# Kernel tuning notes

Hardware: AMD Instinct MI355X
Metric: run time of the kernel (lower is better)

Reference implementation:

```python
import jax, jax.numpy as jnp
import numpy as np

COUPLE_BOOST = 2.0
MARGIN = 1.0
EPS = 1e-6  # both F.normalize eps and F.pairwise_distance eps


def setup_inputs() -> dict:
    key = jax.random.key(0)
    n, d = 8192, 256
    embeddings = jax.random.normal(key, (n, d), dtype=jnp.float32)
    # Alternating couple labels per the is_partner docstring: 0,1,0,1,...
    labels = jnp.tile(jnp.array([0, 1], dtype=jnp.int64), n // 2).reshape(n, 1)
    return {"embeddings": embeddings, "labels": labels}


def reference(embeddings, labels):
    n, d = embeddings.shape
    # F.normalize(p=2, dim=1, eps=1e-6): x / max(||x||, eps)
    norm = jnp.linalg.norm(embeddings, axis=1, keepdims=True)
    e = embeddings / jnp.maximum(norm, EPS)
    # F.pairwise_distance adds eps to the difference: d_ij = ||e_i - e_j + eps||_2
    # ||e_i - e_j + eps*1||^2 = s_i + s_j - 2 G_ij + 2*eps*(r_i - r_j) + d*eps^2
    s = jnp.sum(e * e, axis=1)          # (n,) squared norms
    r = jnp.sum(e, axis=1)              # (n,) row sums
    G = e @ e.T                         # (n, n) gram matrix
    dist2 = (s[:, None] + s[None, :] - 2.0 * G
             + 2.0 * EPS * (r[:, None] - r[None, :]) + d * EPS * EPS)
    dist = jnp.sqrt(jnp.maximum(dist2, 1e-12))

    lab = labels[:, 0]
    idx = jnp.arange(n)
    tril = idx[:, None] > idx[None, :]                  # loop only visits i > j
    same = lab[:, None] == lab[None, :]
    pos_mask = tril & same
    neg_mask = tril & (~same)
    # is_partner with i > j: labels[i]==1 and i == j+1
    partner = (idx[:, None] == idx[None, :] + 1) & (lab[:, None] == 1)
    boost = jnp.where(partner, COUPLE_BOOST, 1.0)

    pos_loss = 0.5 * jnp.square(jnp.maximum(dist - 0.1, 0.0))
    neg_loss = 0.5 * boost * jnp.square(jnp.maximum(MARGIN - dist, 0.0))

    total = (jnp.sum(jnp.where(pos_mask, pos_loss, 0.0))
             + jnp.sum(jnp.where(neg_mask, neg_loss, 0.0)))
    n_comparisons = n * (n - 1) // 2
    return total / n_comparisons
```

## Files before the change

kernel.cpp:

```cpp
#include <hip/hip_runtime.h>
#include <hip/hip_bf16.h>

#define NROWS 8192
#define DIM   256
#define EPSV  1e-6f
#define BM    128
#define BN    128
#define BK    32
#define BKP   40

typedef __bf16 bf16x8 __attribute__((ext_vector_type(8)));
typedef float  f32x4  __attribute__((ext_vector_type(4)));

__global__ __launch_bounds__(256) void normalize_kernel(
    const float* __restrict__ emb, __bf16* __restrict__ Ebf,
    float* __restrict__ P_out, float* __restrict__ Q_out,
    float* __restrict__ out)
{
    if (blockIdx.x == 0 && threadIdx.x == 0) out[0] = 0.0f;

    const int wave = threadIdx.x >> 6;
    const int lane = threadIdx.x & 63;
    const int row  = blockIdx.x * 4 + wave;

    const float4 v = ((const float4*)(emb + row * DIM))[lane];
    float ss = v.x*v.x + v.y*v.y + v.z*v.z + v.w*v.w;
    #pragma unroll
    for (int off = 32; off; off >>= 1) ss += __shfl_xor(ss, off);

    const float inv = 1.0f / fmaxf(sqrtf(ss), EPSV);
    float4 e; e.x = v.x*inv; e.y = v.y*inv; e.z = v.z*inv; e.w = v.w*inv;

    float sp = e.x*e.x + e.y*e.y + e.z*e.z + e.w*e.w;
    float rp = e.x + e.y + e.z + e.w;
    #pragma unroll
    for (int off = 32; off; off >>= 1) {
        sp += __shfl_xor(sp, off);
        rp += __shfl_xor(rp, off);
    }

    union { __bf16 h[4]; uint2 u; } pk;
    pk.h[0] = (__bf16)e.x; pk.h[1] = (__bf16)e.y;
    pk.h[2] = (__bf16)e.z; pk.h[3] = (__bf16)e.w;
    *(uint2*)(Ebf + row * DIM + lane * 4) = pk.u;

    if (lane == 0) {
        const float c = 0.5f * (float)DIM * EPSV * EPSV;
        P_out[row] = sp + 2.0f * EPSV * rp + c;
        Q_out[row] = sp - 2.0f * EPSV * rp + c;
    }
}

__global__ __launch_bounds__(256) void loss_kernel(
    const __bf16* __restrict__ Ebf,
    const float* __restrict__ P_arr, const float* __restrict__ Q_arr,
    const int* __restrict__ lab, float* __restrict__ out)
{
    const int t = blockIdx.x;
    int bi = (int)((sqrtf(8.0f * (float)t + 1.0f) - 1.0f) * 0.5f);
    while ((bi + 1) * (bi + 2) / 2 <= t) ++bi;
    while (bi * (bi + 1) / 2 > t) --bi;
    const int bj = t - bi * (bi + 1) / 2;
    const bool diag = (bi == bj);

    __shared__ __align__(16) __bf16 As[BM * BKP];
    __shared__ __align__(16) __bf16 Bs[BN * BKP];
    __shared__ float sP[BM], sQ[BN];
    __shared__ int   lI[BM], lJ[BN];
    __shared__ float wsum[4];

    const int tid  = threadIdx.x;
    const int wave = tid >> 6;
    const int lane = tid & 63;
    const int i0 = bi * BM, j0 = bj * BN;

    if (tid < 128) {
        sP[tid] = P_arr[i0 + tid]; lI[tid] = lab[i0 + tid];
        sQ[tid] = Q_arr[j0 + tid]; lJ[tid] = lab[j0 + tid];
    }

    f32x4 acc[4][4] = {};
    const int wm = wave >> 1, wn = wave & 1;
    const int quad = lane >> 4, mlane = lane & 15;

    #pragma unroll 1
    for (int kt = 0; kt < DIM / BK; ++kt) {
        const int k0 = kt * BK;
        #pragma unroll
        for (int rr = 0; rr < 2; ++rr) {
            const int c   = tid + rr * 256;
            const int row = c >> 2;
            const int col = (c & 3) * 8;
            *(uint4*)(As + row * BKP + col) =
                *(const uint4*)(Ebf + (size_t)(i0 + row) * DIM + k0 + col);
            *(uint4*)(Bs + row * BKP + col) =
                *(const uint4*)(Ebf + (size_t)(j0 + row) * DIM + k0 + col);
        }
        __syncthreads();

        bf16x8 af[4], bfr[4];
        #pragma unroll
        for (int f = 0; f < 4; ++f) {
            af[f]  = *(const bf16x8*)(As + (wm * 64 + f * 16 + mlane) * BKP + quad * 8);
            bfr[f] = *(const bf16x8*)(Bs + (wn * 64 + f * 16 + mlane) * BKP + quad * 8);
        }
        #pragma unroll
        for (int fa = 0; fa < 4; ++fa)
            #pragma unroll
            for (int fb = 0; fb < 4; ++fb)
                acc[fa][fb] = __builtin_amdgcn_mfma_f32_16x16x32_bf16(
                    af[fa], bfr[fb], acc[fa][fb], 0, 0, 0);
        __syncthreads();
    }

    float qv[4]; int lv[4], gjv[4];
    #pragma unroll
    for (int fb = 0; fb < 4; ++fb) {
        const int jl = wn * 64 + fb * 16 + mlane;
        qv[fb]  = sQ[jl];
        lv[fb]  = lJ[jl];
        gjv[fb] = j0 + jl;
    }

    float lsum = 0.0f;
    #pragma unroll
    for (int fa = 0; fa < 4; ++fa) {
        #pragma unroll
        for (int reg = 0; reg < 4; ++reg) {
            const int il = wm * 64 + fa * 16 + quad * 4 + reg;
            const int gi = i0 + il;
            const float pi = sP[il];
            const int   li = lI[il];
            #pragma unroll
            for (int fb = 0; fb < 4; ++fb) {
                const float g  = acc[fa][fb][reg];
                const float d2 = __builtin_fmaf(-2.0f, g, pi + qv[fb]);
                const float d  = __builtin_amdgcn_sqrtf(fmaxf(d2, 1e-12f));
                const bool same = (li == lv[fb]);
                float tt = same ? (d - 0.1f) : (1.0f - d);
                tt = fmaxf(tt, 0.0f);
                const float w = same ? 0.5f
                                     : ((gi == gjv[fb] + 1 && li == 1) ? 1.0f : 0.5f);
                float contrib = w * tt * tt;
                if (diag) contrib = (gi > gjv[fb]) ? contrib : 0.0f;
                lsum += contrib;
            }
        }
    }

    #pragma unroll
    for (int off = 32; off; off >>= 1) lsum += __shfl_down(lsum, off);
    if (lane == 0) wsum[wave] = lsum;
    __syncthreads();
    if (tid == 0) {
        const float bs = wsum[0] + wsum[1] + wsum[2] + wsum[3];
        const float scale = 1.0f / 33550336.0f;
        atomicAdd(out, bs * scale);
    }
}

extern "C" void kernel_launch(void* const* d_in, const int* in_sizes, int n_in,
                              void* d_out, int out_size, void* d_ws, size_t ws_size,
                              hipStream_t stream)
{
    const float* emb = (const float*)d_in[0];
    const int*   lab = (const int*)d_in[1];
    float*       out = (float*)d_out;

    __bf16* Ebf   = (__bf16*)d_ws;
    float*  P_arr = (float*)((char*)d_ws + (size_t)NROWS * DIM * 2);
    float*  Q_arr = P_arr + NROWS;

    normalize_kernel<<<NROWS / 4, 256, 0, stream>>>(emb, Ebf, P_arr, Q_arr, out);
    loss_kernel<<<64 * 65 / 2, 256, 0, stream>>>(Ebf, P_arr, Q_arr, lab, out);
}
```

Before: 110.1 us.

## Load MFMA fragments directly from global with register double-buffering, drop LDS staging

The loss kernel no longer stages A/B tiles through shared memory with two barriers per k-step. Each wave now loads its bf16x8 fragments straight from global memory and prefetches the next k-slice into registers while the current MFMAs run. Waves whose 64x64 sub-tile lies entirely above the diagonal of a diagonal block skip their work, and P/Q/labels are read from global instead of LDS. The normalize kernel also derives squared norm and row sum from the raw reductions, removing a second shuffle reduction. The trade-off is no cross-wave reuse through LDS, which means more global/L2 traffic and less coalesced loads, plus higher register pressure.

```diff
diff --git a/kernel.cpp b/kernel.cpp
--- a/kernel.cpp
+++ b/kernel.cpp
@@ -4,10 +4,6 @@
 #define NROWS 8192
 #define DIM   256
 #define EPSV  1e-6f
-#define BM    128
-#define BN    128
-#define BK    32
-#define BKP   40
 
 typedef __bf16 bf16x8 __attribute__((ext_vector_type(8)));
 typedef float  f32x4  __attribute__((ext_vector_type(4)));
@@ -25,19 +21,15 @@
 
     const float4 v = ((const float4*)(emb + row * DIM))[lane];
     float ss = v.x*v.x + v.y*v.y + v.z*v.z + v.w*v.w;
+    float rs = v.x + v.y + v.z + v.w;
     #pragma unroll
-    for (int off = 32; off; off >>= 1) ss += __shfl_xor(ss, off);
+    for (int off = 32; off; off >>= 1) {
+        ss += __shfl_xor(ss, off);
+        rs += __shfl_xor(rs, off);
+    }
 
     const float inv = 1.0f / fmaxf(sqrtf(ss), EPSV);
     float4 e; e.x = v.x*inv; e.y = v.y*inv; e.z = v.z*inv; e.w = v.w*inv;
-
-    float sp = e.x*e.x + e.y*e.y + e.z*e.z + e.w*e.w;
-    float rp = e.x + e.y + e.z + e.w;
-    #pragma unroll
-    for (int off = 32; off; off >>= 1) {
-        sp += __shfl_xor(sp, off);
-        rp += __shfl_xor(rp, off);
-    }
 
     union { __bf16 h[4]; uint2 u; } pk;
     pk.h[0] = (__bf16)e.x; pk.h[1] = (__bf16)e.y;
@@ -45,7 +37,9 @@
     *(uint2*)(Ebf + row * DIM + lane * 4) = pk.u;
 
     if (lane == 0) {
-        const float c = 0.5f * (float)DIM * EPSV * EPSV;
+        const float sp = ss * inv * inv;
+        const float rp = rs * inv;
+        const float c  = 0.5f * (float)DIM * EPSV * EPSV;
         P_out[row] = sp + 2.0f * EPSV * rp + c;
         Q_out[row] = sp - 2.0f * EPSV * rp + c;
     }
@@ -63,87 +57,86 @@
     const int bj = t - bi * (bi + 1) / 2;
     const bool diag = (bi == bj);
 
-    __shared__ __align__(16) __bf16 As[BM * BKP];
-    __shared__ __align__(16) __bf16 Bs[BN * BKP];
-    __shared__ float sP[BM], sQ[BN];
-    __shared__ int   lI[BM], lJ[BN];
     __shared__ float wsum[4];
 
     const int tid  = threadIdx.x;
     const int wave = tid >> 6;
     const int lane = tid & 63;
-    const int i0 = bi * BM, j0 = bj * BN;
+    const int i0 = bi * 128, j0 = bj * 128;
 
-    if (tid < 128) {
-        sP[tid] = P_arr[i0 + tid]; lI[tid] = lab[i0 + tid];
-        sQ[tid] = Q_arr[j0 + tid]; lJ[tid] = lab[j0 + tid];
-    }
-
-    f32x4 acc[4][4] = {};
     const int wm = wave >> 1, wn = wave & 1;
     const int quad = lane >> 4, mlane = lane & 15;
 
-    #pragma unroll 1
-    for (int kt = 0; kt < DIM / BK; ++kt) {
-        const int k0 = kt * BK;
-        #pragma unroll
-        for (int rr = 0; rr < 2; ++rr) {
-            const int c   = tid + rr * 256;
-            const int row = c >> 2;
-            const int col = (c & 3) * 8;
-            *(uint4*)(As + row * BKP + col) =
-                *(const uint4*)(Ebf + (size_t)(i0 + row) * DIM + k0 + col);
-            *(uint4*)(Bs + row * BKP + col) =
-                *(const uint4*)(Ebf + (size_t)(j0 + row) * DIM + k0 + col);
-        }
-        __syncthreads();
+    float lsum = 0.0f;
+    const bool skip = diag && (wm < wn);
 
-        bf16x8 af[4], bfr[4];
+    if (!skip) {
+        const __bf16* pA = Ebf + (size_t)(i0 + wm * 64 + mlane) * DIM + quad * 8;
+        const __bf16* pB = Ebf + (size_t)(j0 + wn * 64 + mlane) * DIM + quad * 8;
+
+        f32x4 acc[4][4] = {};
+        bf16x8 a_cur[4], b_cur[4], a_nxt[4], b_nxt[4];
+
         #pragma unroll
         for (int f = 0; f < 4; ++f) {
-            af[f]  = *(const bf16x8*)(As + (wm * 64 + f * 16 + mlane) * BKP + quad * 8);
-            bfr[f] = *(const bf16x8*)(Bs + (wn * 64 + f * 16 + mlane) * BKP + quad * 8);
+            a_cur[f] = *(const bf16x8*)(pA + (size_t)f * 16 * DIM);
+            b_cur[f] = *(const bf16x8*)(pB + (size_t)f * 16 * DIM);
         }
+
         #pragma unroll
-        for (int fa = 0; fa < 4; ++fa)
+        for (int kt = 0; kt < DIM / 32; ++kt) {
+            if (kt < DIM / 32 - 1) {
+                #pragma unroll
+                for (int f = 0; f < 4; ++f) {
+                    a_nxt[f] = *(const bf16x8*)(pA + (size_t)f * 16 * DIM + (kt + 1) * 32);
+                    b_nxt[f] = *(const bf16x8*)(pB + (size_t)f * 16 * DIM + (kt + 1) * 32);
+                }
+            }
             #pragma unroll
-            for (int fb = 0; fb < 4; ++fb)
-                acc[fa][fb] = __builtin_amdgcn_mfma_f32_16x16x32_bf16(
-                    af[fa], bfr[fb], acc[fa][fb], 0, 0, 0);
-        __syncthreads();
-    }
+            for (int fa = 0; fa < 4; ++fa)
+                #pragma unroll
+                for (int fb = 0; fb < 4; ++fb)
+                    acc[fa][fb] = __builtin_amdgcn_mfma_f32_16x16x32_bf16(
+                        a_cur[fa], b_cur[fb], acc[fa][fb], 0, 0, 0);
+            #pragma unroll
+            for (int f = 0; f < 4; ++f) { a_cur[f] = a_nxt[f]; b_cur[f] = b_nxt[f]; }
+        }
 
-    float qv[4]; int lv[4], gjv[4];
-    #pragma unroll
-    for (int fb = 0; fb < 4; ++fb) {
-        const int jl = wn * 64 + fb * 16 + mlane;
-        qv[fb]  = sQ[jl];
-        lv[fb]  = lJ[jl];
-        gjv[fb] = j0 + jl;
-    }
+        float qv[4]; int lv[4], gjv[4];
+        #pragma unroll
+        for (int fb = 0; fb < 4; ++fb) {
+            const int jl = wn * 64 + fb * 16 + mlane;
+            qv[fb]  = Q_arr[j0 + jl];
+            lv[fb]  = lab[j0 + jl];
+            gjv[fb] = j0 + jl;
+        }
 
-    float lsum = 0.0f;
-    #pragma unroll
-    for (int fa = 0; fa < 4; ++fa) {
         #pragma unroll
-        for (int reg = 0; reg < 4; ++reg) {
-            const int il = wm * 64 + fa * 16 + quad * 4 + reg;
-            const int gi = i0 + il;
-            const float pi = sP[il];
-            const int   li = lI[il];
+        for (int fa = 0; fa < 4; ++fa) {
+            const int ibase = i0 + wm * 64 + fa * 16 + quad * 4;
+            const float4 pv  = *(const float4*)(P_arr + ibase);
+            const int4   liv = *(const int4*)(lab + ibase);
             #pragma unroll
-            for (int fb = 0; fb < 4; ++fb) {
-                const float g  = acc[fa][fb][reg];
-                const float d2 = __builtin_fmaf(-2.0f, g, pi + qv[fb]);
-                const float d  = __builtin_amdgcn_sqrtf(fmaxf(d2, 1e-12f));
-                const bool same = (li == lv[fb]);
-                float tt = same ? (d - 0.1f) : (1.0f - d);
-                tt = fmaxf(tt, 0.0f);
-                const float w = same ? 0.5f
-                                     : ((gi == gjv[fb] + 1 && li == 1) ? 1.0f : 0.5f);
-                float contrib = w * tt * tt;
-                if (diag) contrib = (gi > gjv[fb]) ? contrib : 0.0f;
-                lsum += contrib;
+            for (int reg = 0; reg < 4; ++reg) {
+                const int gi = ibase + reg;
+                const float pi = (reg == 0) ? pv.x : (reg == 1) ? pv.y
+                               : (reg == 2) ? pv.z : pv.w;
+                const int li   = (reg == 0) ? liv.x : (reg == 1) ? liv.y
+                               : (reg == 2) ? liv.z : liv.w;
+                #pragma unroll
+                for (int fb = 0; fb < 4; ++fb) {
+                    const float g  = acc[fa][fb][reg];
+                    const float d2 = __builtin_fmaf(-2.0f, g, pi + qv[fb]);
+                    const float d  = __builtin_amdgcn_sqrtf(fmaxf(d2, 1e-12f));
+                    const bool same = (li == lv[fb]);
+                    float tt = same ? (d - 0.1f) : (1.0f - d);
+                    tt = fmaxf(tt, 0.0f);
+                    const float w = same ? 0.5f
+                                         : ((gi == gjv[fb] + 1 && li == 1) ? 1.0f : 0.5f);
+                    float contrib = w * tt * tt;
+                    if (diag) contrib = (gi > gjv[fb]) ? contrib : 0.0f;
+                    lsum += contrib;
+                }
             }
         }
     }
```

Result: slower. 145.1 us (+31.7%).
